# Performance work log

Hardware: AMD Instinct MI355X
Metric: run time of the kernel (lower is better)

The kernel has to match this reference:

```python
import jax, jax.numpy as jnp
import numpy as np

N = 80000
E = 1280000
EPS = 1e-5

def _lrelu(x):
    return jax.nn.leaky_relu(x, 0.01)

def _bn(h):
    # training-mode BatchNorm1d with batch size 1: stats over the node dim; affine is identity at init
    return (h - h.mean(0)) / jnp.sqrt(h.var(0) + EPS)

def _ln(h, g, b):
    m = h.mean(-1, keepdims=True)
    v = h.var(-1, keepdims=True)
    return (h - m) / jnp.sqrt(v + EPS) * g + b

def _gcn(h, w, b, src, dst, n):
    # PyG GCNConv: add self loops, symmetric deg^-1/2 normalization, aggregate at target
    hw = h @ w.T
    loop = jnp.arange(n, dtype=src.dtype)
    s = jnp.concatenate([src, loop])
    d = jnp.concatenate([dst, loop])
    deg = jax.ops.segment_sum(jnp.ones(d.shape, hw.dtype), d, num_segments=n)
    dinv = jnp.where(deg > 0, 1.0 / jnp.sqrt(deg), 0.0)
    msg = hw[s] * (dinv[s] * dinv[d])[:, None]  # [E+N, C]
    return jax.ops.segment_sum(msg, d, num_segments=n) + b

def _tnet(x, c1w, c1b, c2w, c2b, c3w, c3b, f1w, f1b, f2w, f2b, f3w, f3b):
    h = jax.nn.relu(x @ c1w.T + c1b)          # [N,64]  (source skips bn1)
    h = jax.nn.relu(_bn(h @ c2w.T + c2b))     # [N,128]
    h = jax.nn.relu(_bn(h @ c3w.T + c3b))     # [N,1024]
    g = h.max(0)                              # global max pool -> [1024]
    g = jax.nn.relu(g @ f1w.T + f1b)
    g = jax.nn.relu(g @ f2w.T + f2b)
    iden = jnp.array([1.0, 0.0, 0.0, 0.0, 1.0, 0.0, 0.0, 0.0, 1.0], x.dtype)
    g = g @ f3w.T + f3b + iden
    return g.reshape(3, 3)

def _forward(edge_index, x, tnet_c1_w, tnet_c1_b, tnet_c2_w, tnet_c2_b, tnet_c3_w, tnet_c3_b, tnet_fc1_w, tnet_fc1_b, tnet_fc2_w, tnet_fc2_b, tnet_fc3_w, tnet_fc3_b, conv1_w, conv1_b, g1_li_w, g1_li_b, g1_gcn_w, g1_gcn_b, g1_ln_g, g1_ln_b, conv2_w, conv2_b, g2_li_w, g2_li_b, g2_gcn_w, g2_gcn_b, g2_ln_g, g2_ln_b, conv3_w, conv3_b, out_w, out_b):
    src, dst = edge_index[0], edge_index[1]
    n = x.shape[0]
    T = _tnet(x, tnet_c1_w, tnet_c1_b, tnet_c2_w, tnet_c2_b, tnet_c3_w, tnet_c3_b, tnet_fc1_w, tnet_fc1_b, tnet_fc2_w, tnet_fc2_b, tnet_fc3_w, tnet_fc3_b)
    h0 = x @ T                                  # [N,3] spatial transform
    xg = _lrelu(h0 @ conv1_w.T + conv1_b)       # [N,64] (conv1d k=1 == per-node linear)
    # Gcn_Attention 1
    nf = _lrelu(xg @ g1_li_w.T + g1_li_b)
    nf2 = _lrelu(_gcn(nf, g1_gcn_w, g1_gcn_b, src, dst, n))
    h = _ln(jnp.concatenate([nf, nf2], 1), g1_ln_g, g1_ln_b)   # [N,128]
    h = _lrelu(h @ conv2_w.T + conv2_b)
    # Gcn_Attention 2
    nf = _lrelu(h @ g2_li_w.T + g2_li_b)
    nf2 = _lrelu(_gcn(nf, g2_gcn_w, g2_gcn_b, src, dst, n))
    h = _ln(jnp.concatenate([nf, nf2], 1), g2_ln_g, g2_ln_b)   # [N,256]
    h = jnp.concatenate([h, xg], 1)                            # [N,320]
    h = _lrelu(h @ conv3_w.T + conv3_b)                        # [N,256]
    pooled = h.mean(0)                                         # global mean pool (single graph)
    feat = jnp.concatenate([jnp.broadcast_to(pooled, (n, pooled.shape[0])), xg], 1)  # [N,320]
    return feat @ out_w.T + out_b                              # [N,4]

def setup_inputs():
    ki = iter(jax.random.split(jax.random.key(0), 32))
    def W(shape):
        return jax.random.normal(next(ki), shape, jnp.float32) * (1.0 / float(np.sqrt(shape[-1])))
    z = lambda n: jnp.zeros((n,), jnp.float32)
    o = lambda n: jnp.ones((n,), jnp.float32)
    inp = {}
    inp['x'] = jax.random.normal(next(ki), (N, 3), jnp.float32)
    inp['edge_index'] = jax.random.randint(next(ki), (2, E), 0, N, dtype=jnp.int32)
    inp['tnet_c1_w'] = W((64, 3)); inp['tnet_c1_b'] = z(64)
    inp['tnet_c2_w'] = W((128, 64)); inp['tnet_c2_b'] = z(128)
    inp['tnet_c3_w'] = W((1024, 128)); inp['tnet_c3_b'] = z(1024)
    inp['tnet_fc1_w'] = W((512, 1024)); inp['tnet_fc1_b'] = z(512)
    inp['tnet_fc2_w'] = W((256, 512)); inp['tnet_fc2_b'] = z(256)
    inp['tnet_fc3_w'] = W((9, 256)); inp['tnet_fc3_b'] = z(9)
    inp['conv1_w'] = W((64, 3)); inp['conv1_b'] = z(64)
    inp['g1_li_w'] = W((64, 64)); inp['g1_li_b'] = z(64)
    inp['g1_gcn_w'] = W((64, 64)); inp['g1_gcn_b'] = z(64)
    inp['g1_ln_g'] = o(128); inp['g1_ln_b'] = z(128)
    inp['conv2_w'] = W((128, 128)); inp['conv2_b'] = z(128)
    inp['g2_li_w'] = W((128, 128)); inp['g2_li_b'] = z(128)
    inp['g2_gcn_w'] = W((128, 128)); inp['g2_gcn_b'] = z(128)
    inp['g2_ln_g'] = o(256); inp['g2_ln_b'] = z(256)
    inp['conv3_w'] = W((256, 320)); inp['conv3_b'] = z(256)
    inp['out_w'] = W((4, 320)); inp['out_b'] = z(4)
    return inp

def reference(x, edge_index, tnet_c1_w, tnet_c1_b, tnet_c2_w, tnet_c2_b, tnet_c3_w, tnet_c3_b, tnet_fc1_w, tnet_fc1_b, tnet_fc2_w, tnet_fc2_b, tnet_fc3_w, tnet_fc3_b, conv1_w, conv1_b, g1_li_w, g1_li_b, g1_gcn_w, g1_gcn_b, g1_ln_g, g1_ln_b, conv2_w, conv2_b, g2_li_w, g2_li_b, g2_gcn_w, g2_gcn_b, g2_ln_g, g2_ln_b, conv3_w, conv3_b, out_w, out_b):
    return _forward(edge_index, x, tnet_c1_w, tnet_c1_b, tnet_c2_w, tnet_c2_b, tnet_c3_w, tnet_c3_b, tnet_fc1_w, tnet_fc1_b, tnet_fc2_w, tnet_fc2_b, tnet_fc3_w, tnet_fc3_b, conv1_w, conv1_b, g1_li_w, g1_li_b, g1_gcn_w, g1_gcn_b, g1_ln_g, g1_ln_b, conv2_w, conv2_b, g2_li_w, g2_li_b, g2_gcn_w, g2_gcn_b, g2_ln_g, g2_ln_b, conv3_w, conv3_b, out_w, out_b)
```

## Files before the change

### kernel.cpp

```cpp
#include <hip/hip_runtime.h>
#include <cstddef>

#define EPSV 1e-5f

typedef __attribute__((ext_vector_type(8))) short frag8;
typedef __attribute__((ext_vector_type(4))) float f32x4;

__device__ __forceinline__ float lrelu01(float v) { return v > 0.f ? v : 0.01f * v; }
__device__ __forceinline__ void atomAddF(float* p, float v) { unsafeAtomicAdd(p, v); }
__device__ __forceinline__ unsigned fkey(float f) {
    unsigned u = __float_as_uint(f);
    return (u & 0x80000000u) ? ~u : (u | 0x80000000u);
}
__device__ __forceinline__ unsigned short f2b(float f) {
    unsigned u = __float_as_uint(f);
    unsigned r = u + 0x7fffu + ((u >> 16) & 1u);
    return (unsigned short)(r >> 16);
}
__device__ __forceinline__ float b2f(unsigned short h) {
    return __uint_as_float(((unsigned)h) << 16);
}
__device__ __forceinline__ float blo(unsigned u) { return __uint_as_float(u << 16); }
__device__ __forceinline__ float bhi(unsigned u) { return __uint_as_float(u & 0xffff0000u); }

static inline unsigned cdivu(unsigned a, unsigned b) { return (a + b - 1) / b; }


__global__ void k_degrank(const int* __restrict__ dst, int* __restrict__ deg,
                          int* __restrict__ rank, int E) {
    int e = blockIdx.x * 256 + threadIdx.x;
    if (e < E) rank[e] = atomicAdd(&deg[dst[e]], 1);
}

__global__ void k_dinv(const int* __restrict__ deg, float* __restrict__ dinv, int n) {
    int i = blockIdx.x * 256 + threadIdx.x;
    if (i < n) dinv[i] = rsqrtf((float)(deg[i] + 1));
}

__global__ void k_scan_local(const int* __restrict__ deg, int* __restrict__ startv,
                             int* __restrict__ bsum, int n) {
    __shared__ int t0[256];
    int tid = threadIdx.x;
    int i = blockIdx.x * 256 + tid;
    int v = (i < n) ? deg[i] : 0;
    t0[tid] = v;
    __syncthreads();
    for (int o = 1; o < 256; o <<= 1) {
        int add = (tid >= o) ? t0[tid - o] : 0;
        __syncthreads();
        t0[tid] += add;
        __syncthreads();
    }
    if (i < n) startv[i] = t0[tid] - v;
    if (tid == 255) bsum[blockIdx.x] = t0[255];
}

__global__ void k_scan_bsum(int* __restrict__ bsum, int nb) {
    __shared__ int t0[512];
    int tid = threadIdx.x;
    int v = (tid < nb) ? bsum[tid] : 0;
    t0[tid] = v;
    __syncthreads();
    for (int o = 1; o < 512; o <<= 1) {
        int add = (tid >= o) ? t0[tid - o] : 0;
        __syncthreads();
        t0[tid] += add;
        __syncthreads();
    }
    if (tid < nb) bsum[tid] = t0[tid] - v;
}

__global__ void k_scan_add(int* __restrict__ startv, const int* __restrict__ bsum, int n) {
    int i = blockIdx.x * 256 + threadIdx.x;
    if (i < n) startv[i] += bsum[blockIdx.x];
}

__global__ void k_fill(const int* __restrict__ src, const int* __restrict__ dst,
                       const int* __restrict__ rank, const int* __restrict__ startv,
                       int* __restrict__ csr, int E) {
    int e = blockIdx.x * 256 + threadIdx.x;
    if (e < E) csr[startv[dst[e]] + rank[e]] = src[e];
}

template <int CH>
__launch_bounds__(256)
__global__ void k_gln(const int* __restrict__ startv, const int* __restrict__ degv,
                      const int* __restrict__ csr, const unsigned short* __restrict__ q,
                      const unsigned short* __restrict__ nf, const float* __restrict__ dinv,
                      const float* __restrict__ gcn_b, const float* __restrict__ lng,
                      const float* __restrict__ lnb, unsigned short* __restrict__ outp,
                      int ldo, int n) {
    const int wv = threadIdx.x >> 6, lane = threadIdx.x & 63;
    const int g = lane >> 4, p = lane & 15;
    int node = blockIdx.x * 4 + wv;
    if (node >= n) return;
    constexpr int CPL = CH / 16;
    constexpr int DPL = CPL / 2;

    float acc[CPL];
#pragma unroll
    for (int k = 0; k < CPL; ++k) acc[k] = 0.f;

    {
        unsigned su[DPL];
        const unsigned short* qrow = q + (size_t)node * CH + p * CPL;
        if (DPL == 4) *(uint4*)su = *(const uint4*)qrow;
        else          *(uint2*)su = *(const uint2*)qrow;
        if (g == 0) {
#pragma unroll
            for (int d = 0; d < DPL; ++d) { acc[2 * d] += blo(su[d]); acc[2 * d + 1] += bhi(su[d]); }
        }
    }

    int s0 = startv[node], cnt = degv[node];
    int sidx[4];
#pragma unroll
    for (int t = 0; t < 4; ++t) { int j = t * 4 + g; sidx[t] = (j < cnt) ? csr[s0 + j] : 0; }
    for (int j0 = 0; j0 < cnt; j0 += 16) {
        unsigned buf[4][DPL];
#pragma unroll
        for (int t = 0; t < 4; ++t) {
            const unsigned short* src = q + (size_t)sidx[t] * CH + p * CPL;
            if (DPL == 4) *(uint4*)buf[t] = *(const uint4*)src;
            else          *(uint2*)buf[t] = *(const uint2*)src;
        }
        int nsidx[4];
#pragma unroll
        for (int t = 0; t < 4; ++t) {
            int j = j0 + 16 + t * 4 + g;
            nsidx[t] = (j < cnt) ? csr[s0 + j] : 0;
        }
#pragma unroll
        for (int t = 0; t < 4; ++t) {
            if (j0 + t * 4 + g < cnt) {
#pragma unroll
                for (int d = 0; d < DPL; ++d) {
                    acc[2 * d] += blo(buf[t][d]);
                    acc[2 * d + 1] += bhi(buf[t][d]);
                }
            }
        }
#pragma unroll
        for (int t = 0; t < 4; ++t) sidx[t] = nsidx[t];
    }

#pragma unroll
    for (int k = 0; k < CPL; ++k) {
        acc[k] += __shfl_xor(acc[k], 16);
        acc[k] += __shfl_xor(acc[k], 32);
    }

    float di = dinv[node];
    float nv[CPL], bv[CPL];
    {
        unsigned su[DPL];
        const unsigned short* nrow = nf + (size_t)node * CH + p * CPL;
        if (DPL == 4) *(uint4*)su = *(const uint4*)nrow;
        else          *(uint2*)su = *(const uint2*)nrow;
#pragma unroll
        for (int d = 0; d < DPL; ++d) { nv[2 * d] = blo(su[d]); nv[2 * d + 1] = bhi(su[d]); }
    }
    const float* gb = gcn_b + p * CPL;
#pragma unroll
    for (int k = 0; k < CPL; ++k) bv[k] = lrelu01(di * acc[k] + gb[k]);

    float s = 0.f, ss = 0.f;
#pragma unroll
    for (int k = 0; k < CPL; ++k) { s += nv[k] + bv[k]; ss += nv[k] * nv[k] + bv[k] * bv[k]; }
#pragma unroll
    for (int off = 32; off > 0; off >>= 1) { s += __shfl_xor(s, off); ss += __shfl_xor(ss, off); }
    const float inv = 1.f / (float)(8 * CH);
    float mu = s * inv;
    float var = ss * inv - mu * mu;
    float rsg = rsqrtf(var + EPSV);

    unsigned short* orow = outp + (size_t)node * ldo;
    if (g == 0) {
        unsigned short tmp[CPL];
        const float* lg = lng + p * CPL; const float* lb = lnb + p * CPL;
#pragma unroll
        for (int k = 0; k < CPL; ++k) tmp[k] = f2b((nv[k] - mu) * rsg * lg[k] + lb[k]);
        if (DPL == 4) *(uint4*)(orow + p * CPL) = *(uint4*)tmp;
        else          *(uint2*)(orow + p * CPL) = *(uint2*)tmp;
    } else if (g == 1) {
        unsigned short tmp[CPL];
        const float* lg = lng + CH + p * CPL; const float* lb = lnb + CH + p * CPL;
#pragma unroll
        for (int k = 0; k < CPL; ++k) tmp[k] = f2b((bv[k] - mu) * rsg * lg[k] + lb[k]);
        if (DPL == 4) *(uint4*)(orow + CH + p * CPL) = *(uint4*)tmp;
        else          *(uint2*)(orow + CH + p * CPL) = *(uint2*)tmp;
    }
}


__global__ void k_wconv(const float* __restrict__ s0, const float* __restrict__ s1,
                        const float* __restrict__ s2, const float* __restrict__ s3,
                        const float* __restrict__ s4, const float* __restrict__ s5,
                        const float* __restrict__ s6, const float* __restrict__ s7,
                        unsigned short* __restrict__ dst) {
    int t = blockIdx.x * 256 + threadIdx.x;
    if (t >= 278528) return;
    const float* srcs[8] = {s0, s1, s2, s3, s4, s5, s6, s7};
    const int off[9] = {0, 8192, 139264, 143360, 147456, 163840, 180224, 196608, 278528};
    int seg = 0;
    while (t >= off[seg + 1]) ++seg;
    dst[t] = f2b(srcs[seg][t - off[seg]]);
}

__global__ void k_h1(const float* __restrict__ x, const float* __restrict__ w,
                     const float* __restrict__ b, unsigned short* __restrict__ h1, int n) {
    int node = blockIdx.x * 256 + threadIdx.x;
    if (node >= n) return;
    float x0 = x[node * 3], x1 = x[node * 3 + 1], x2 = x[node * 3 + 2];
    unsigned short* o = h1 + (size_t)node * 64;
#pragma unroll
    for (int cp = 0; cp < 8; ++cp) {
        unsigned short tmp[8];
#pragma unroll
        for (int t = 0; t < 8; ++t) {
            int c = cp * 8 + t;
            float v = x0 * w[c * 3] + x1 * w[c * 3 + 1] + x2 * w[c * 3 + 2] + b[c];
            tmp[t] = f2b(fmaxf(v, 0.f));
        }
        *(float4*)(o + cp * 8) = *(float4*)tmp;
    }
}

__global__ void k_murs(const float* __restrict__ sum2, const float* __restrict__ ss2,
                       float* __restrict__ mu2, float* __restrict__ rs2, float invn) {
    int c = threadIdx.x;
    float m = sum2[c] * invn;
    float var = ss2[c] * invn - m * m;
    mu2[c] = m;
    rs2[c] = rsqrtf(var + EPSV);
}

__global__ void k_prebn(const float* __restrict__ z, const float* __restrict__ mu,
                        const float* __restrict__ rs, unsigned short* __restrict__ a3,
                        int total) {
    int t = (blockIdx.x * 256 + threadIdx.x) * 4;
    if (t >= total) return;
    int c = t & 127;
    float4 v = *(const float4*)(z + t);
    ushort4 o;
    o.x = f2b(fmaxf((v.x - mu[c + 0]) * rs[c + 0], 0.f));
    o.y = f2b(fmaxf((v.y - mu[c + 1]) * rs[c + 1], 0.f));
    o.z = f2b(fmaxf((v.z - mu[c + 2]) * rs[c + 2], 0.f));
    o.w = f2b(fmaxf((v.w - mu[c + 3]) * rs[c + 3], 0.f));
    *(ushort4*)(a3 + t) = o;
}

__global__ void k_g(const float* __restrict__ sum3, const float* __restrict__ ss3,
                    const unsigned* __restrict__ maxk, float* __restrict__ g, float invn) {
    int c = blockIdx.x * 256 + threadIdx.x;
    float m = sum3[c] * invn;
    float var = ss3[c] * invn - m * m;
    unsigned k = maxk[c];
    unsigned u = (k & 0x80000000u) ? (k & 0x7FFFFFFFu) : ~k;
    g[c] = fmaxf((__uint_as_float(u) - m) * rsqrtf(var + EPSV), 0.f);
}

__global__ void k_fc1(const float* __restrict__ g, const float* __restrict__ f1w,
                      const float* __restrict__ f1b, float* __restrict__ a1) {
    int row = blockIdx.x * 64 + (threadIdx.x >> 2);
    int part = threadIdx.x & 3;
    const float* w = f1w + (size_t)row * 1024 + part * 256;
    const float* gg = g + part * 256;
    float s = 0.f;
    for (int k = 0; k < 256; ++k) s = fmaf(w[k], gg[k], s);
    s += __shfl_xor(s, 1); s += __shfl_xor(s, 2);
    if (part == 0) a1[row] = fmaxf(s + f1b[row], 0.f);
}

__launch_bounds__(256)
__global__ void k_fc23(const float* __restrict__ a1, const float* __restrict__ f2w,
                       const float* __restrict__ f2b, const float* __restrict__ f3w,
                       const float* __restrict__ f3b, float* __restrict__ T9) {
    __shared__ float a2[256];
    int tid = threadIdx.x;
    {
        const float* w = f2w + (size_t)tid * 512;
        float s = f2b[tid];
        for (int k = 0; k < 512; ++k) s = fmaf(w[k], a1[k], s);
        a2[tid] = fmaxf(s, 0.f);
    }
    __syncthreads();
    if (tid < 9) {
        const float* w = f3w + (size_t)tid * 256;
        float s = f3b[tid];
        for (int k = 0; k < 256; ++k) s = fmaf(w[k], a2[k], s);
        if (tid == 0 || tid == 4 || tid == 8) s += 1.f;
        T9[tid] = s;
    }
}

__global__ void k_xg(const float* __restrict__ x, const float* __restrict__ T9,
                     const float* __restrict__ w, const float* __restrict__ b,
                     unsigned short* __restrict__ xg, int n) {
    int node = blockIdx.x * 256 + threadIdx.x;
    if (node >= n) return;
    float x0 = x[node * 3], x1 = x[node * 3 + 1], x2 = x[node * 3 + 2];
    float h0 = x0 * T9[0] + x1 * T9[3] + x2 * T9[6];
    float h1 = x0 * T9[1] + x1 * T9[4] + x2 * T9[7];
    float h2 = x0 * T9[2] + x1 * T9[5] + x2 * T9[8];
    unsigned short* o = xg + (size_t)node * 320;
#pragma unroll
    for (int cp = 0; cp < 8; ++cp) {
        unsigned short tmp[8];
#pragma unroll
        for (int t = 0; t < 8; ++t) {
            int c = cp * 8 + t;
            float v = h0 * w[c * 3] + h1 * w[c * 3 + 1] + h2 * w[c * 3 + 2] + b[c];
            tmp[t] = f2b(lrelu01(v));
        }
        *(float4*)(o + cp * 8) = *(float4*)tmp;
    }
}

__global__ void k_const4(const float* __restrict__ pooled, const float* __restrict__ ow,
                         const float* __restrict__ ob, float* __restrict__ c4, float invn) {
    int j = threadIdx.x >> 6, lane = threadIdx.x & 63;
    float s = 0.f;
    for (int c = lane; c < 256; c += 64) s += pooled[c] * invn * ow[j * 320 + c];
#pragma unroll
    for (int off = 32; off > 0; off >>= 1) s += __shfl_down(s, off);
    if (lane == 0) c4[j] = s + ob[j];
}

__global__ void k_out(const unsigned short* __restrict__ hcat, const float* __restrict__ ow,
                      const float* __restrict__ c4, float* __restrict__ out, int n) {
    int node = blockIdx.x * 256 + threadIdx.x;
    if (node >= n) return;
    const unsigned short* xgp = hcat + (size_t)node * 320 + 256;
    float s0 = c4[0], s1 = c4[1], s2 = c4[2], s3 = c4[3];
#pragma unroll
    for (int cp = 0; cp < 8; ++cp) {
        float4 raw = *(const float4*)(xgp + cp * 8);
        unsigned short tmp[8];
        *(float4*)tmp = raw;
#pragma unroll
        for (int t = 0; t < 8; ++t) {
            int k = 256 + cp * 8 + t;
            float f = b2f(tmp[t]);
            s0 = fmaf(f, ow[k], s0);
            s1 = fmaf(f, ow[320 + k], s1);
            s2 = fmaf(f, ow[640 + k], s2);
            s3 = fmaf(f, ow[960 + k], s3);
        }
    }
    *(float4*)(out + (size_t)node * 4) = make_float4(s0, s1, s2, s3);
}

enum { MF_BIAS = 1, MF_LRELU = 2, MF_DINV = 4, MF_STOREF = 8, MF_STOREB = 16,
       MF_STATS = 32, MF_COLSUM = 64 };

template <int BN, int MODE>
__launch_bounds__(256)
__global__ void k_mgemm(const unsigned short* __restrict__ A, int lda, int K,
                        const unsigned short* __restrict__ W,
                        const float* __restrict__ bias,
                        float* __restrict__ OutF, unsigned short* __restrict__ OutB, int ldo,
                        const float* __restrict__ dinv,
                        float* __restrict__ sum_o, float* __restrict__ ss_o,
                        unsigned* __restrict__ maxk_o) {
    constexpr int BM = 128;
    constexpr int LDT = 40;
    __shared__ unsigned short As[BM * LDT];
    __shared__ unsigned short Ws[BN * LDT];
    __shared__ float redS[2 * 128];
    __shared__ unsigned redM[128];

    const int tid = threadIdx.x;
    const int wid = tid >> 6, lane = tid & 63;
    const int quad = lane >> 4, lrow = lane & 15;
    const int bn0 = blockIdx.x * BM;
    const int bc0 = blockIdx.y * BN;

    constexpr int NI = (BN == 128) ? 4 : 2;
    constexpr int NJ = 4;
    const int wm = (BN == 128) ? (wid & 1) * 64 : wid * 32;
    const int wn = (BN == 128) ? (wid >> 1) * 64 : 0;

    if (MODE & (MF_STATS | MF_COLSUM)) {
        for (int c = tid; c < BN; c += 256) {
            redS[c] = 0.f; redS[128 + c] = 0.f; redM[c] = 0u;
        }
    }

    f32x4 acc[NI][NJ] = {};

    for (int k0 = 0; k0 < K; k0 += 32) {
#pragma unroll
        for (int h = 0; h < 2; ++h) {
            int ch = tid + h * 256;
            int row = ch >> 2, cp = ch & 3;
            const unsigned short* src = A + (size_t)(bn0 + row) * lda + k0 + cp * 8;
            *(float4*)&As[row * LDT + cp * 8] = *(const float4*)src;
        }
#pragma unroll
        for (int h = 0; h < BN / 64; ++h) {
            int ch = tid + h * 256;
            int row = ch >> 2, cp = ch & 3;
            const unsigned short* src = W + (size_t)(bc0 + row) * K + k0 + cp * 8;
            *(float4*)&Ws[row * LDT + cp * 8] = *(const float4*)src;
        }
        __syncthreads();
        frag8 af[NI], bf[NJ];
#pragma unroll
        for (int i = 0; i < NI; ++i)
            af[i] = *(const frag8*)&As[(wm + i * 16 + lrow) * LDT + quad * 8];
#pragma unroll
        for (int j = 0; j < NJ; ++j)
            bf[j] = *(const frag8*)&Ws[(wn + j * 16 + lrow) * LDT + quad * 8];
#pragma unroll
        for (int i = 0; i < NI; ++i)
#pragma unroll
            for (int j = 0; j < NJ; ++j)
                acc[i][j] = __builtin_amdgcn_mfma_f32_16x16x32_bf16(af[i], bf[j], acc[i][j], 0, 0, 0);
        __syncthreads();
    }

#pragma unroll
    for (int j = 0; j < NJ; ++j) {
        const int col = bc0 + wn + j * 16 + lrow;
        float bv = (MODE & MF_BIAS) ? bias[col] : 0.f;
        float s = 0.f, q = 0.f, m = -3.4e38f;
#pragma unroll
        for (int i = 0; i < NI; ++i) {
            const int rowb = bn0 + wm + i * 16 + quad * 4;
#pragma unroll
            for (int r = 0; r < 4; ++r) {
                float t = acc[i][j][r] + bv;
                if (MODE & MF_LRELU) t = lrelu01(t);
                if (MODE & MF_DINV) t *= dinv[rowb + r];
                if (MODE & MF_STOREF) OutF[(size_t)(rowb + r) * ldo + col] = t;
                if (MODE & MF_STOREB) OutB[(size_t)(rowb + r) * ldo + col] = f2b(t);
                s += t; q += t * t; m = fmaxf(m, t);
            }
        }
        if (MODE & (MF_STATS | MF_COLSUM)) {
            s += __shfl_xor(s, 16); s += __shfl_xor(s, 32);
            if (MODE & MF_STATS) {
                q += __shfl_xor(q, 16); q += __shfl_xor(q, 32);
                m = fmaxf(m, __shfl_xor(m, 16)); m = fmaxf(m, __shfl_xor(m, 32));
            }
            if (quad == 0) {
                int lc = wn + j * 16 + lrow;
                atomicAdd(&redS[lc], s);
                if (MODE & MF_STATS) {
                    atomicAdd(&redS[128 + lc], q);
                    atomicMax(&redM[lc], fkey(m));
                }
            }
        }
    }
    if (MODE & (MF_STATS | MF_COLSUM)) {
        __syncthreads();
        for (int c = tid; c < BN; c += 256) {
            atomAddF(&sum_o[bc0 + c], redS[c]);
            if (MODE & MF_STATS) {
                atomAddF(&ss_o[bc0 + c], redS[128 + c]);
                atomicMax(&maxk_o[bc0 + c], redM[c]);
            }
        }
    }
}

template <int BN>
__launch_bounds__(256)
__global__ void k_ligc(const unsigned short* __restrict__ A, int lda, int K,
                       const unsigned short* __restrict__ Wli, const float* __restrict__ bli,
                       const unsigned short* __restrict__ Wgc, const float* __restrict__ dinv,
                       unsigned short* __restrict__ NF, int ldnf,
                       unsigned short* __restrict__ Q, int ldq) {
    constexpr int BM = 128;
    constexpr int LDT = 40;
    constexpr int LDT2 = BN + 8;
    __shared__ unsigned short SA[BM * LDT2];
    __shared__ unsigned short Ws[BN * LDT];

    const int tid = threadIdx.x;
    const int wid = tid >> 6, lane = tid & 63;
    const int quad = lane >> 4, lrow = lane & 15;
    const int bn0 = blockIdx.x * BM;
    constexpr int NI = (BN == 128) ? 4 : 2;
    constexpr int NJ = 4;
    const int wm = (BN == 128) ? (wid & 1) * 64 : wid * 32;
    const int wn = (BN == 128) ? (wid >> 1) * 64 : 0;

    {
        f32x4 acc[NI][NJ] = {};
        for (int k0 = 0; k0 < K; k0 += 32) {
#pragma unroll
            for (int h = 0; h < 2; ++h) {
                int ch = tid + h * 256;
                int row = ch >> 2, cp = ch & 3;
                *(float4*)&SA[row * LDT + cp * 8] =
                    *(const float4*)(A + (size_t)(bn0 + row) * lda + k0 + cp * 8);
            }
#pragma unroll
            for (int h = 0; h < BN / 64; ++h) {
                int ch = tid + h * 256;
                int row = ch >> 2, cp = ch & 3;
                *(float4*)&Ws[row * LDT + cp * 8] =
                    *(const float4*)(Wli + (size_t)row * K + k0 + cp * 8);
            }
            __syncthreads();
            frag8 af[NI], bf[NJ];
#pragma unroll
            for (int i = 0; i < NI; ++i)
                af[i] = *(const frag8*)&SA[(wm + i * 16 + lrow) * LDT + quad * 8];
#pragma unroll
            for (int j = 0; j < NJ; ++j)
                bf[j] = *(const frag8*)&Ws[(wn + j * 16 + lrow) * LDT + quad * 8];
#pragma unroll
            for (int i = 0; i < NI; ++i)
#pragma unroll
                for (int j = 0; j < NJ; ++j)
                    acc[i][j] = __builtin_amdgcn_mfma_f32_16x16x32_bf16(af[i], bf[j], acc[i][j], 0, 0, 0);
            __syncthreads();
        }
#pragma unroll
        for (int j = 0; j < NJ; ++j) {
            const int col = wn + j * 16 + lrow;
            float bv = bli[col];
#pragma unroll
            for (int i = 0; i < NI; ++i) {
                const int rowl = wm + i * 16 + quad * 4;
#pragma unroll
                for (int r = 0; r < 4; ++r) {
                    unsigned short h = f2b(lrelu01(acc[i][j][r] + bv));
                    NF[(size_t)(bn0 + rowl + r) * ldnf + col] = h;
                    SA[(rowl + r) * LDT2 + col] = h;
                }
            }
        }
        __syncthreads();
    }
    {
        f32x4 acc[NI][NJ] = {};
        for (int k0 = 0; k0 < BN; k0 += 32) {
#pragma unroll
            for (int h = 0; h < BN / 64; ++h) {
                int ch = tid + h * 256;
                int row = ch >> 2, cp = ch & 3;
                *(float4*)&Ws[row * LDT + cp * 8] =
                    *(const float4*)(Wgc + (size_t)row * BN + k0 + cp * 8);
            }
            __syncthreads();
            frag8 af[NI], bf[NJ];
#pragma unroll
            for (int i = 0; i < NI; ++i)
                af[i] = *(const frag8*)&SA[(wm + i * 16 + lrow) * LDT2 + k0 + quad * 8];
#pragma unroll
            for (int j = 0; j < NJ; ++j)
                bf[j] = *(const frag8*)&Ws[(wn + j * 16 + lrow) * LDT + quad * 8];
#pragma unroll
            for (int i = 0; i < NI; ++i)
#pragma unroll
                for (int j = 0; j < NJ; ++j)
                    acc[i][j] = __builtin_amdgcn_mfma_f32_16x16x32_bf16(af[i], bf[j], acc[i][j], 0, 0, 0);
            __syncthreads();
        }
#pragma unroll
        for (int j = 0; j < NJ; ++j) {
            const int col = wn + j * 16 + lrow;
#pragma unroll
            for (int i = 0; i < NI; ++i) {
                const int rowb = bn0 + wm + i * 16 + quad * 4;
#pragma unroll
                for (int r = 0; r < 4; ++r) {
                    float t = acc[i][j][r] * dinv[rowb + r];
                    Q[(size_t)(rowb + r) * ldq + col] = f2b(t);
                }
            }
        }
    }
}

__launch_bounds__(256)
__global__ void k_z3(const unsigned short* __restrict__ A,
                     const unsigned short* __restrict__ W,
                     const float* __restrict__ bias,
                     float* __restrict__ sum_o, float* __restrict__ ss_o,
                     unsigned* __restrict__ maxk_o) {
    constexpr int LDT = 40;
    __shared__ unsigned short As[4 * 128 * LDT];
    __shared__ unsigned short Ws[128 * LDT];
    __shared__ float redS[2 * 128];
    __shared__ unsigned redM[128];

    const int tid = threadIdx.x;
    const int wid = tid >> 6, lane = tid & 63;
    const int quad = lane >> 4, lrow = lane & 15;
    const int bn0 = blockIdx.x * 128;
    const int wm = (wid & 1) * 64;
    const int wn = (wid >> 1) * 64;

#pragma unroll
    for (int h = 0; h < 8; ++h) {
        int ch = tid + h * 256;
        int row = ch >> 4, cp = ch & 15, kc = cp >> 2, sub = cp & 3;
        *(float4*)&As[kc * 128 * LDT + row * LDT + sub * 8] =
            *(const float4*)(A + (size_t)(bn0 + row) * 128 + cp * 8);
    }

    for (int cb = 0; cb < 8; ++cb) {
        f32x4 acc[4][4] = {};
        for (int kc = 0; kc < 4; ++kc) {
            __syncthreads();
#pragma unroll
            for (int h = 0; h < 2; ++h) {
                int ch = tid + h * 256;
                int row = ch >> 2, sub = ch & 3;
                *(float4*)&Ws[row * LDT + sub * 8] =
                    *(const float4*)(W + (size_t)(cb * 128 + row) * 128 + kc * 32 + sub * 8);
            }
            __syncthreads();
            frag8 af[4], bf[4];
#pragma unroll
            for (int i = 0; i < 4; ++i)
                af[i] = *(const frag8*)&As[kc * 128 * LDT + (wm + i * 16 + lrow) * LDT + quad * 8];
#pragma unroll
            for (int j = 0; j < 4; ++j)
                bf[j] = *(const frag8*)&Ws[(wn + j * 16 + lrow) * LDT + quad * 8];
#pragma unroll
            for (int i = 0; i < 4; ++i)
#pragma unroll
                for (int j = 0; j < 4; ++j)
                    acc[i][j] = __builtin_amdgcn_mfma_f32_16x16x32_bf16(af[i], bf[j], acc[i][j], 0, 0, 0);
        }
        __syncthreads();
        for (int c = tid; c < 128; c += 256) {
            redS[c] = 0.f; redS[128 + c] = 0.f; redM[c] = 0u;
        }
        __syncthreads();
#pragma unroll
        for (int j = 0; j < 4; ++j) {
            int lc = wn + j * 16 + lrow;
            float bv = bias[cb * 128 + lc];
            float s = 0.f, q = 0.f, m = -3.4e38f;
#pragma unroll
            for (int i = 0; i < 4; ++i)
#pragma unroll
                for (int r = 0; r < 4; ++r) {
                    float t = acc[i][j][r] + bv;
                    s += t; q += t * t; m = fmaxf(m, t);
                }
            s += __shfl_xor(s, 16); s += __shfl_xor(s, 32);
            q += __shfl_xor(q, 16); q += __shfl_xor(q, 32);
            m = fmaxf(m, __shfl_xor(m, 16)); m = fmaxf(m, __shfl_xor(m, 32));
            if (quad == 0) {
                atomicAdd(&redS[lc], s);
                atomicAdd(&redS[128 + lc], q);
                atomicMax(&redM[lc], fkey(m));
            }
        }
        __syncthreads();
        for (int c = tid; c < 128; c += 256) {
            atomAddF(&sum_o[cb * 128 + c], redS[c]);
            atomAddF(&ss_o[cb * 128 + c], redS[128 + c]);
            atomicMax(&maxk_o[cb * 128 + c], redM[c]);
        }
    }
}


extern "C" void kernel_launch(void* const* d_in, const int* in_sizes, int n_in,
                              void* d_out, int out_size, void* d_ws, size_t ws_size,
                              hipStream_t stream) {
    const float* x   = (const float*)d_in[0];
    const int*   ei  = (const int*)d_in[1];
    const float* c1w = (const float*)d_in[2];  const float* c1b = (const float*)d_in[3];
    const float* c2w = (const float*)d_in[4];  const float* c2b = (const float*)d_in[5];
    const float* c3w = (const float*)d_in[6];  const float* c3b = (const float*)d_in[7];
    const float* f1w = (const float*)d_in[8];  const float* f1b = (const float*)d_in[9];
    const float* f2w = (const float*)d_in[10]; const float* f2b = (const float*)d_in[11];
    const float* f3w = (const float*)d_in[12]; const float* f3b = (const float*)d_in[13];
    const float* cv1w = (const float*)d_in[14]; const float* cv1b = (const float*)d_in[15];
    const float* li1w = (const float*)d_in[16]; const float* li1b = (const float*)d_in[17];
    const float* gc1w = (const float*)d_in[18]; const float* gc1b = (const float*)d_in[19];
    const float* ln1g = (const float*)d_in[20]; const float* ln1b = (const float*)d_in[21];
    const float* cv2w = (const float*)d_in[22]; const float* cv2b = (const float*)d_in[23];
    const float* li2w = (const float*)d_in[24]; const float* li2b = (const float*)d_in[25];
    const float* gc2w = (const float*)d_in[26]; const float* gc2b = (const float*)d_in[27];
    const float* ln2g = (const float*)d_in[28]; const float* ln2b = (const float*)d_in[29];
    const float* cv3w = (const float*)d_in[30]; const float* cv3b = (const float*)d_in[31];
    const float* ow  = (const float*)d_in[32]; const float* ob  = (const float*)d_in[33];
    float* out = (float*)d_out;

    const int N = in_sizes[0] / 3;
    const int E = in_sizes[1] / 2;
    const int* srcI = ei;
    const int* dstI = ei + E;

    char* base = (char*)d_ws;
    size_t off = 0;
    auto take = [&](size_t bytes) -> char* {
        char* p = base + off;
        off = (off + bytes + 255) & ~(size_t)255;
        return p;
    };
    int*   deg    = (int*)  take((size_t)N * 4);
    float* dinv   = (float*)take((size_t)N * 4);
    int*   startv = (int*)  take((size_t)N * 4);
    int*   rank   = (int*)  take((size_t)E * 4);
    int*   csr    = (int*)  take((size_t)E * 4);
    int*   bsum   = (int*)  take(512 * 4);
    float* sm     = (float*)take(8192 * 4);
    unsigned short* WB = (unsigned short*)take(278528 * 2);
    unsigned short* H  = (unsigned short*)take((size_t)N * 320 * 2);
    float* F1 = (float*)take((size_t)N * 128 * 4);
    unsigned short* B1 = (unsigned short*)take((size_t)N * 64 * 2);
    unsigned short* B2 = (unsigned short*)take((size_t)N * 128 * 2);
    unsigned short* B3 = (unsigned short*)take((size_t)N * 128 * 2);

    unsigned short* c2wb  = WB + 0;
    unsigned short* c3wb  = WB + 8192;
    unsigned short* li1wb = WB + 139264;
    unsigned short* gc1wb = WB + 143360;
    unsigned short* cv2wb = WB + 147456;
    unsigned short* li2wb = WB + 163840;
    unsigned short* gc2wb = WB + 180224;
    unsigned short* cv3wb = WB + 196608;

    float* sum2 = sm + 0;    float* ss2 = sm + 128;
    float* sum3 = sm + 256;  float* ss3 = sm + 1280;
    unsigned* maxk = (unsigned*)(sm + 2304);
    float* pooled = sm + 3328;
    unsigned* dmax = (unsigned*)(sm + 3584);
    float* mu2 = sm + 3712; float* rs2 = sm + 3840;
    float* T9  = sm + 3968; float* c4 = sm + 3984;
    float* gbuf = sm + 4096;
    float* a1   = sm + 5120;

    const float invn = 1.0f / (float)N;
    const dim3 blk(256);
    const unsigned GX = (unsigned)(N / 128);
    const unsigned NB = cdivu((unsigned)N, 256);

    hipMemsetAsync(deg, 0, (size_t)N * 4, stream);
    hipMemsetAsync(sm, 0, 3712 * 4, stream);

    k_degrank<<<cdivu(E, 256), blk, 0, stream>>>(dstI, deg, rank, E);
    k_dinv<<<cdivu(N, 256), blk, 0, stream>>>(deg, dinv, N);
    k_scan_local<<<NB, blk, 0, stream>>>(deg, startv, bsum, N);
    k_scan_bsum<<<1, 512, 0, stream>>>(bsum, (int)NB);
    k_scan_add<<<NB, blk, 0, stream>>>(startv, bsum, N);
    k_fill<<<cdivu(E, 256), blk, 0, stream>>>(srcI, dstI, rank, startv, csr, E);

    k_wconv<<<cdivu(278528, 256), blk, 0, stream>>>(c2w, c3w, li1w, gc1w, cv2w, li2w, gc2w, cv3w, WB);

    k_h1<<<cdivu((unsigned)N, 256), blk, 0, stream>>>(x, c1w, c1b, B1, N);
    k_mgemm<128, (MF_BIAS | MF_STOREF | MF_STATS)><<<dim3(GX, 1), blk, 0, stream>>>(
        B1, 64, 64, c2wb, c2b, F1, nullptr, 128, nullptr, sum2, ss2, dmax);
    k_murs<<<1, 128, 0, stream>>>(sum2, ss2, mu2, rs2, invn);
    k_prebn<<<cdivu((unsigned)N * 128 / 4, 256), blk, 0, stream>>>(F1, mu2, rs2, B2, N * 128);
    k_z3<<<GX, blk, 0, stream>>>(B2, c3wb, c3b, sum3, ss3, maxk);
    k_g<<<4, blk, 0, stream>>>(sum3, ss3, maxk, gbuf, invn);
    k_fc1<<<8, blk, 0, stream>>>(gbuf, f1w, f1b, a1);
    k_fc23<<<1, blk, 0, stream>>>(a1, f2w, f2b, f3w, f3b, T9);
    k_xg<<<cdivu((unsigned)N, 256), blk, 0, stream>>>(x, T9, cv1w, cv1b, H + 256, N);

    k_ligc<64><<<GX, blk, 0, stream>>>(H + 256, 320, 64, li1wb, li1b, gc1wb, dinv, B1, 64, B2, 64);
    k_gln<64><<<cdivu((unsigned)N, 4), blk, 0, stream>>>(
        startv, deg, csr, B2, B1, dinv, gc1b, ln1g, ln1b, B3, 128, N);
    k_mgemm<128, (MF_BIAS | MF_LRELU | MF_STOREB)><<<dim3(GX, 1), blk, 0, stream>>>(
        B3, 128, 128, cv2wb, cv2b, nullptr, B2, 128, nullptr, nullptr, nullptr, nullptr);

    k_ligc<128><<<GX, blk, 0, stream>>>(B2, 128, 128, li2wb, li2b, gc2wb, dinv, B3, 128, B2, 128);
    k_gln<128><<<cdivu((unsigned)N, 4), blk, 0, stream>>>(
        startv, deg, csr, B2, B3, dinv, gc2b, ln2g, ln2b, H, 320, N);

    k_mgemm<128, (MF_BIAS | MF_LRELU | MF_COLSUM)><<<dim3(GX, 2), blk, 0, stream>>>(
        H, 320, 320, cv3wb, cv3b, nullptr, nullptr, 0, nullptr, pooled, nullptr, nullptr);

    k_const4<<<1, 256, 0, stream>>>(pooled, ow, ob, c4, invn);
    k_out<<<cdivu((unsigned)N, 256), blk, 0, stream>>>(H, ow, c4, out, N);
}
```

Measured before the change: 582.6 us.

## Fuse BN-normalize into z3 GEMM, deepen mgemm K-tile, restructure z3 tiling

Removes the separate pre-BN kernel: k_z3 now reads the fp32 pre-activation, applies BN and ReLU and converts to bf16 while staging A into shared memory, which avoids a full write and re-read of an N×128 bf16 buffer. k_z3 is also retiled to hold the whole K=128 A tile once and loop over 16 output-column blocks of 64, with global atomics per column instead of block-level shared reduction. k_mgemm processes K in steps of 64 rather than 32, halving the number of barriers per tile. The trade-offs are more global atomic traffic in z3, larger shared-memory use, and a K multiple of 64 assumption in mgemm (the K values used are 64, 128 and 320, and 320 is a multiple of 64).

Result: slower. 608.5 us (+4.4%).

```diff
diff --git a/kernel.cpp b/kernel.cpp
--- a/kernel.cpp
+++ b/kernel.cpp
@@ -235,21 +235,6 @@
     rs2[c] = rsqrtf(var + EPSV);
 }
 
-__global__ void k_prebn(const float* __restrict__ z, const float* __restrict__ mu,
-                        const float* __restrict__ rs, unsigned short* __restrict__ a3,
-                        int total) {
-    int t = (blockIdx.x * 256 + threadIdx.x) * 4;
-    if (t >= total) return;
-    int c = t & 127;
-    float4 v = *(const float4*)(z + t);
-    ushort4 o;
-    o.x = f2b(fmaxf((v.x - mu[c + 0]) * rs[c + 0], 0.f));
-    o.y = f2b(fmaxf((v.y - mu[c + 1]) * rs[c + 1], 0.f));
-    o.z = f2b(fmaxf((v.z - mu[c + 2]) * rs[c + 2], 0.f));
-    o.w = f2b(fmaxf((v.w - mu[c + 3]) * rs[c + 3], 0.f));
-    *(ushort4*)(a3 + t) = o;
-}
-
 __global__ void k_g(const float* __restrict__ sum3, const float* __restrict__ ss3,
                     const unsigned* __restrict__ maxk, float* __restrict__ g, float invn) {
     int c = blockIdx.x * 256 + threadIdx.x;
@@ -364,7 +349,7 @@
                         float* __restrict__ sum_o, float* __restrict__ ss_o,
                         unsigned* __restrict__ maxk_o) {
     constexpr int BM = 128;
-    constexpr int LDT = 40;
+    constexpr int LDT = 72;
     __shared__ unsigned short As[BM * LDT];
     __shared__ unsigned short Ws[BN * LDT];
     __shared__ float redS[2 * 128];
@@ -389,34 +374,37 @@
 
     f32x4 acc[NI][NJ] = {};
 
-    for (int k0 = 0; k0 < K; k0 += 32) {
-#pragma unroll
-        for (int h = 0; h < 2; ++h) {
+    for (int k0 = 0; k0 < K; k0 += 64) {
+#pragma unroll
+        for (int h = 0; h < 4; ++h) {
             int ch = tid + h * 256;
-            int row = ch >> 2, cp = ch & 3;
-            const unsigned short* src = A + (size_t)(bn0 + row) * lda + k0 + cp * 8;
-            *(float4*)&As[row * LDT + cp * 8] = *(const float4*)src;
-        }
-#pragma unroll
-        for (int h = 0; h < BN / 64; ++h) {
+            int row = ch >> 3, cp = ch & 7;
+            *(float4*)&As[row * LDT + cp * 8] =
+                *(const float4*)(A + (size_t)(bn0 + row) * lda + k0 + cp * 8);
+        }
+#pragma unroll
+        for (int h = 0; h < BN / 32; ++h) {
             int ch = tid + h * 256;
-            int row = ch >> 2, cp = ch & 3;
-            const unsigned short* src = W + (size_t)(bc0 + row) * K + k0 + cp * 8;
-            *(float4*)&Ws[row * LDT + cp * 8] = *(const float4*)src;
-        }
-        __syncthreads();
-        frag8 af[NI], bf[NJ];
-#pragma unroll
-        for (int i = 0; i < NI; ++i)
-            af[i] = *(const frag8*)&As[(wm + i * 16 + lrow) * LDT + quad * 8];
-#pragma unroll
-        for (int j = 0; j < NJ; ++j)
-            bf[j] = *(const frag8*)&Ws[(wn + j * 16 + lrow) * LDT + quad * 8];
-#pragma unroll
-        for (int i = 0; i < NI; ++i)
+            int row = ch >> 3, cp = ch & 7;
+            *(float4*)&Ws[row * LDT + cp * 8] =
+                *(const float4*)(W + (size_t)(bc0 + row) * K + k0 + cp * 8);
+        }
+        __syncthreads();
+#pragma unroll
+        for (int kc = 0; kc < 2; ++kc) {
+            frag8 af[NI], bf[NJ];
+#pragma unroll
+            for (int i = 0; i < NI; ++i)
+                af[i] = *(const frag8*)&As[(wm + i * 16 + lrow) * LDT + kc * 32 + quad * 8];
 #pragma unroll
             for (int j = 0; j < NJ; ++j)
-                acc[i][j] = __builtin_amdgcn_mfma_f32_16x16x32_bf16(af[i], bf[j], acc[i][j], 0, 0, 0);
+                bf[j] = *(const frag8*)&Ws[(wn + j * 16 + lrow) * LDT + kc * 32 + quad * 8];
+#pragma unroll
+            for (int i = 0; i < NI; ++i)
+#pragma unroll
+                for (int j = 0; j < NJ; ++j)
+                    acc[i][j] = __builtin_amdgcn_mfma_f32_16x16x32_bf16(af[i], bf[j], acc[i][j], 0, 0, 0);
+        }
         __syncthreads();
     }
 
@@ -579,66 +567,72 @@
 }
 
 __launch_bounds__(256)
-__global__ void k_z3(const unsigned short* __restrict__ A,
+__global__ void k_z3(const float* __restrict__ Z, const float* __restrict__ mu,
+                     const float* __restrict__ rs,
                      const unsigned short* __restrict__ W,
                      const float* __restrict__ bias,
                      float* __restrict__ sum_o, float* __restrict__ ss_o,
                      unsigned* __restrict__ maxk_o) {
-    constexpr int LDT = 40;
-    __shared__ unsigned short As[4 * 128 * LDT];
-    __shared__ unsigned short Ws[128 * LDT];
-    __shared__ float redS[2 * 128];
-    __shared__ unsigned redM[128];
+    constexpr int LDT = 136;
+    __shared__ unsigned short As[128 * LDT];
+    __shared__ unsigned short Ws[64 * LDT];
 
     const int tid = threadIdx.x;
     const int wid = tid >> 6, lane = tid & 63;
     const int quad = lane >> 4, lrow = lane & 15;
     const int bn0 = blockIdx.x * 128;
     const int wm = (wid & 1) * 64;
-    const int wn = (wid >> 1) * 64;
+    const int wn = (wid >> 1) * 32;
 
 #pragma unroll
     for (int h = 0; h < 8; ++h) {
         int ch = tid + h * 256;
-        int row = ch >> 4, cp = ch & 15, kc = cp >> 2, sub = cp & 3;
-        *(float4*)&As[kc * 128 * LDT + row * LDT + sub * 8] =
-            *(const float4*)(A + (size_t)(bn0 + row) * 128 + cp * 8);
-    }
-
-    for (int cb = 0; cb < 8; ++cb) {
-        f32x4 acc[4][4] = {};
+        int row = ch >> 4, cp = ch & 15;
+        const float* src = Z + (size_t)(bn0 + row) * 128 + cp * 8;
+        float4 v0 = *(const float4*)src;
+        float4 v1 = *(const float4*)(src + 4);
+        int c = cp * 8;
+        unsigned short t[8];
+        t[0] = f2b(fmaxf((v0.x - mu[c + 0]) * rs[c + 0], 0.f));
+        t[1] = f2b(fmaxf((v0.y - mu[c + 1]) * rs[c + 1], 0.f));
+        t[2] = f2b(fmaxf((v0.z - mu[c + 2]) * rs[c + 2], 0.f));
+        t[3] = f2b(fmaxf((v0.w - mu[c + 3]) * rs[c + 3], 0.f));
+        t[4] = f2b(fmaxf((v1.x - mu[c + 4]) * rs[c + 4], 0.f));
+        t[5] = f2b(fmaxf((v1.y - mu[c + 5]) * rs[c + 5], 0.f));
+        t[6] = f2b(fmaxf((v1.z - mu[c + 6]) * rs[c + 6], 0.f));
+        t[7] = f2b(fmaxf((v1.w - mu[c + 7]) * rs[c + 7], 0.f));
+        *(float4*)&As[row * LDT + cp * 8] = *(float4*)t;
+    }
+
+    for (int cb = 0; cb < 16; ++cb) {
+#pragma unroll
+        for (int h = 0; h < 4; ++h) {
+            int ch = tid + h * 256;
+            int row = ch >> 4, cp = ch & 15;
+            *(float4*)&Ws[row * LDT + cp * 8] =
+                *(const float4*)(W + (size_t)(cb * 64 + row) * 128 + cp * 8);
+        }
+        __syncthreads();
+        f32x4 acc[4][2] = {};
+#pragma unroll
         for (int kc = 0; kc < 4; ++kc) {
-            __syncthreads();
-#pragma unroll
-            for (int h = 0; h < 2; ++h) {
-                int ch = tid + h * 256;
-                int row = ch >> 2, sub = ch & 3;
-                *(float4*)&Ws[row * LDT + sub * 8] =
-                    *(const float4*)(W + (size_t)(cb * 128 + row) * 128 + kc * 32 + sub * 8);
-            }
-            __syncthreads();
-            frag8 af[4], bf[4];
+            frag8 af[4], bf[2];
 #pragma unroll
             for (int i = 0; i < 4; ++i)
-                af[i] = *(const frag8*)&As[kc * 128 * LDT + (wm + i * 16 + lrow) * LDT + quad * 8];
-#pragma unroll
-            for (int j = 0; j < 4; ++j)
-                bf[j] = *(const frag8*)&Ws[(wn + j * 16 + lrow) * LDT + quad * 8];
+                af[i] = *(const frag8*)&As[(wm + i * 16 + lrow) * LDT + kc * 32 + quad * 8];
+#pragma unroll
+            for (int j = 0; j < 2; ++j)
+                bf[j] = *(const frag8*)&Ws[(wn + j * 16 + lrow) * LDT + kc * 32 + quad * 8];
 #pragma unroll
             for (int i = 0; i < 4; ++i)
 #pragma unroll
-                for (int j = 0; j < 4; ++j)
+                for (int j = 0; j < 2; ++j)
                     acc[i][j] = __builtin_amdgcn_mfma_f32_16x16x32_bf16(af[i], bf[j], acc[i][j], 0, 0, 0);
         }
-        __syncthreads();
-        for (int c = tid; c < 128; c += 256) {
-            redS[c] = 0.f; redS[128 + c] = 0.f; redM[c] = 0u;
-        }
-        __syncthreads();
-#pragma unroll
-        for (int j = 0; j < 4; ++j) {
-            int lc = wn + j * 16 + lrow;
-            float bv = bias[cb * 128 + lc];
+#pragma unroll
+        for (int j = 0; j < 2; ++j) {
+            int c = cb * 64 + wn + j * 16 + lrow;
+            float bv = bias[c];
             float s = 0.f, q = 0.f, m = -3.4e38f;
 #pragma unroll
             for (int i = 0; i < 4; ++i)
@@ -651,17 +645,12 @@
             q += __shfl_xor(q, 16); q += __shfl_xor(q, 32);
             m = fmaxf(m, __shfl_xor(m, 16)); m = fmaxf(m, __shfl_xor(m, 32));
             if (quad == 0) {
-                atomicAdd(&redS[lc], s);
-                atomicAdd(&redS[128 + lc], q);
-                atomicMax(&redM[lc], fkey(m));
-            }
-        }
-        __syncthreads();
-        for (int c = tid; c < 128; c += 256) {
-            atomAddF(&sum_o[cb * 128 + c], redS[c]);
-            atomAddF(&ss_o[cb * 128 + c], redS[128 + c]);
-            atomicMax(&maxk_o[cb * 128 + c], redM[c]);
-        }
+                atomAddF(&sum_o[c], s);
+                atomAddF(&ss_o[c], q);
+                atomicMax(&maxk_o[c], fkey(m));
+            }
+        }
+        __syncthreads();
     }
 }
 
@@ -755,8 +744,7 @@
     k_mgemm<128, (MF_BIAS | MF_STOREF | MF_STATS)><<<dim3(GX, 1), blk, 0, stream>>>(
         B1, 64, 64, c2wb, c2b, F1, nullptr, 128, nullptr, sum2, ss2, dmax);
     k_murs<<<1, 128, 0, stream>>>(sum2, ss2, mu2, rs2, invn);
-    k_prebn<<<cdivu((unsigned)N * 128 / 4, 256), blk, 0, stream>>>(F1, mu2, rs2, B2, N * 128);
-    k_z3<<<GX, blk, 0, stream>>>(B2, c3wb, c3b, sum3, ss3, maxk);
+    k_z3<<<GX, blk, 0, stream>>>(F1, mu2, rs2, c3wb, c3b, sum3, ss3, maxk);
     k_g<<<4, blk, 0, stream>>>(sum3, ss3, maxk, gbuf, invn);
     k_fc1<<<8, blk, 0, stream>>>(gbuf, f1w, f1b, a1);
     k_fc23<<<1, blk, 0, stream>>>(a1, f2w, f2b, f3w, f3b, T9);
```

## Split k_z3 column blocks across grid and pre-swizzle tiles for MFMA fragments

Applied to the files above, without the earlier changes.

The T-net conv3 stats kernel used to loop over eight 128-column output blocks inside each block, reloading weight chunks with barriers every k-step. Now the grid is 2D (8 column blocks × node tiles), each block loads its full 128x128 A and W tiles once into LDS in a fragment-ordered layout, and runs the MFMAs with no inner barriers. Per-column sum, sum of squares and max now go straight to global atomics from each wave instead of through an LDS reduction. This trades 8x more blocks, 8x more reads of the A tile and more global atomic traffic for much more parallelism and fewer syncs.

Result: no change. 575.4 us (-1.2%).

```diff
diff --git a/kernel.cpp b/kernel.cpp
--- a/kernel.cpp
+++ b/kernel.cpp
@@ -584,83 +584,62 @@
                      const float* __restrict__ bias,
                      float* __restrict__ sum_o, float* __restrict__ ss_o,
                      unsigned* __restrict__ maxk_o) {
-    constexpr int LDT = 40;
-    __shared__ unsigned short As[4 * 128 * LDT];
-    __shared__ unsigned short Ws[128 * LDT];
-    __shared__ float redS[2 * 128];
-    __shared__ unsigned redM[128];
-
+    __shared__ unsigned short As[128 * 128];
+    __shared__ unsigned short Ws[128 * 128];
     const int tid = threadIdx.x;
     const int wid = tid >> 6, lane = tid & 63;
     const int quad = lane >> 4, lrow = lane & 15;
-    const int bn0 = blockIdx.x * 128;
-    const int wm = (wid & 1) * 64;
-    const int wn = (wid >> 1) * 64;
+    const int bn0 = blockIdx.y * 128;
+    const int bc0 = blockIdx.x * 128;
 
 #pragma unroll
     for (int h = 0; h < 8; ++h) {
-        int ch = tid + h * 256;
-        int row = ch >> 4, cp = ch & 15, kc = cp >> 2, sub = cp & 3;
-        *(float4*)&As[kc * 128 * LDT + row * LDT + sub * 8] =
-            *(const float4*)(A + (size_t)(bn0 + row) * 128 + cp * 8);
-    }
-
-    for (int cb = 0; cb < 8; ++cb) {
-        f32x4 acc[4][4] = {};
-        for (int kc = 0; kc < 4; ++kc) {
-            __syncthreads();
-#pragma unroll
-            for (int h = 0; h < 2; ++h) {
-                int ch = tid + h * 256;
-                int row = ch >> 2, sub = ch & 3;
-                *(float4*)&Ws[row * LDT + sub * 8] =
-                    *(const float4*)(W + (size_t)(cb * 128 + row) * 128 + kc * 32 + sub * 8);
-            }
-            __syncthreads();
-            frag8 af[4], bf[4];
-#pragma unroll
-            for (int i = 0; i < 4; ++i)
-                af[i] = *(const frag8*)&As[kc * 128 * LDT + (wm + i * 16 + lrow) * LDT + quad * 8];
+        int flat = h * 256 + tid;
+        int l = flat & 63, kc = (flat >> 6) & 3, r16 = flat >> 8;
+        int row = r16 * 16 + (l & 15), k0 = kc * 32 + (l >> 4) * 8;
+        *(float4*)&As[flat * 8] = *(const float4*)(A + (size_t)(bn0 + row) * 128 + k0);
+        *(float4*)&Ws[flat * 8] = *(const float4*)(W + (size_t)(bc0 + row) * 128 + k0);
+    }
+    __syncthreads();
+
+    const int ar = (wid & 1) * 4;
+    const int wc = (wid >> 1) * 4;
+    f32x4 acc[4][4] = {};
+#pragma unroll
+    for (int kc = 0; kc < 4; ++kc) {
+        frag8 af[4], bf[4];
+#pragma unroll
+        for (int i = 0; i < 4; ++i)
+            af[i] = *(const frag8*)&As[(((ar + i) * 4 + kc) * 64 + lane) * 8];
+#pragma unroll
+        for (int j = 0; j < 4; ++j)
+            bf[j] = *(const frag8*)&Ws[(((wc + j) * 4 + kc) * 64 + lane) * 8];
+#pragma unroll
+        for (int i = 0; i < 4; ++i)
 #pragma unroll
             for (int j = 0; j < 4; ++j)
-                bf[j] = *(const frag8*)&Ws[(wn + j * 16 + lrow) * LDT + quad * 8];
-#pragma unroll
-            for (int i = 0; i < 4; ++i)
-#pragma unroll
-                for (int j = 0; j < 4; ++j)
-                    acc[i][j] = __builtin_amdgcn_mfma_f32_16x16x32_bf16(af[i], bf[j], acc[i][j], 0, 0, 0);
-        }
-        __syncthreads();
-        for (int c = tid; c < 128; c += 256) {
-            redS[c] = 0.f; redS[128 + c] = 0.f; redM[c] = 0u;
-        }
-        __syncthreads();
-#pragma unroll
-        for (int j = 0; j < 4; ++j) {
-            int lc = wn + j * 16 + lrow;
-            float bv = bias[cb * 128 + lc];
-            float s = 0.f, q = 0.f, m = -3.4e38f;
-#pragma unroll
-            for (int i = 0; i < 4; ++i)
-#pragma unroll
-                for (int r = 0; r < 4; ++r) {
-                    float t = acc[i][j][r] + bv;
-                    s += t; q += t * t; m = fmaxf(m, t);
-                }
-            s += __shfl_xor(s, 16); s += __shfl_xor(s, 32);
-            q += __shfl_xor(q, 16); q += __shfl_xor(q, 32);
-            m = fmaxf(m, __shfl_xor(m, 16)); m = fmaxf(m, __shfl_xor(m, 32));
-            if (quad == 0) {
-                atomicAdd(&redS[lc], s);
-                atomicAdd(&redS[128 + lc], q);
-                atomicMax(&redM[lc], fkey(m));
-            }
-        }
-        __syncthreads();
-        for (int c = tid; c < 128; c += 256) {
-            atomAddF(&sum_o[cb * 128 + c], redS[c]);
-            atomAddF(&ss_o[cb * 128 + c], redS[128 + c]);
-            atomicMax(&maxk_o[cb * 128 + c], redM[c]);
+                acc[i][j] = __builtin_amdgcn_mfma_f32_16x16x32_bf16(af[i], bf[j], acc[i][j], 0, 0, 0);
+    }
+
+#pragma unroll
+    for (int j = 0; j < 4; ++j) {
+        int c = bc0 + (wc + j) * 16 + lrow;
+        float bv = bias[c];
+        float s = 0.f, q = 0.f, m = -3.4e38f;
+#pragma unroll
+        for (int i = 0; i < 4; ++i)
+#pragma unroll
+            for (int r = 0; r < 4; ++r) {
+                float t = acc[i][j][r] + bv;
+                s += t; q += t * t; m = fmaxf(m, t);
+            }
+        s += __shfl_xor(s, 16); s += __shfl_xor(s, 32);
+        q += __shfl_xor(q, 16); q += __shfl_xor(q, 32);
+        m = fmaxf(m, __shfl_xor(m, 16)); m = fmaxf(m, __shfl_xor(m, 32));
+        if (quad == 0) {
+            atomAddF(&sum_o[c], s);
+            atomAddF(&ss_o[c], q);
+            atomicMax(&maxk_o[c], fkey(m));
         }
     }
 }
@@ -756,7 +735,7 @@
         B1, 64, 64, c2wb, c2b, F1, nullptr, 128, nullptr, sum2, ss2, dmax);
     k_murs<<<1, 128, 0, stream>>>(sum2, ss2, mu2, rs2, invn);
     k_prebn<<<cdivu((unsigned)N * 128 / 4, 256), blk, 0, stream>>>(F1, mu2, rs2, B2, N * 128);
-    k_z3<<<GX, blk, 0, stream>>>(B2, c3wb, c3b, sum3, ss3, maxk);
+    k_z3<<<dim3(8, GX), blk, 0, stream>>>(B2, c3wb, c3b, sum3, ss3, maxk);
     k_g<<<4, blk, 0, stream>>>(sum3, ss3, maxk, gbuf, invn);
     k_fc1<<<8, blk, 0, stream>>>(gbuf, f1w, f1b, a1);
     k_fc23<<<1, blk, 0, stream>>>(a1, f2w, f2b, f3w, f3b, T9);
```
